# Optimization experiments

Hardware: AMD Instinct MI355X
Metric: run time of the kernel (lower is better)

## Reference

```python
import jax, jax.numpy as jnp
import numpy as np

# Config constants (match init_kwargs)
T = 1024            # num_tokens
H = 2048            # hidden_size
E = 16              # n_routed_experts
I = 1408            # moe_intermediate_size
TOP_K = 4           # num_experts_per_tok
N_GROUP = 4         # n_group
TOPK_GROUP = 2      # topk_group
N_SHARED = 2        # n_shared_experts
SI = I * N_SHARED   # shared intermediate = 2816
ROUTED_SCALE = 1.0  # routed_scaling_factor
RENORMALIZE = True  # norm_topk_prob


def setup_inputs() -> dict:
    key = jax.random.key(0)
    ks = jax.random.split(key, 6)
    scale_w = 0.02  # keep router logits in a sane range
    return {
        "x": jax.random.normal(ks[0], (T, H), dtype=jnp.float32),
        "gate_w": jax.random.normal(ks[1], (E, H), dtype=jnp.float32) * scale_w,
        "w_gate_up": jax.random.normal(ks[2], (E, H, 2 * I), dtype=jnp.float32) * scale_w,
        "w_down": jax.random.normal(ks[3], (E, I, H), dtype=jnp.float32) * scale_w,
        "shared_gate_up": jax.random.normal(ks[4], (H, 2 * SI), dtype=jnp.float32) * scale_w,
        "shared_down": jax.random.normal(ks[5], (SI, H), dtype=jnp.float32) * scale_w,
    }


def _silu_and_mul(gu):
    gate, up = jnp.split(gu, 2, axis=-1)
    return jax.nn.silu(gate) * up


def _grouped_topk(logits):
    # scores over experts, grouped top-k group selection, then top-k experts
    scores = jax.nn.softmax(logits, axis=-1)                          # [T, E]
    group_scores = scores.reshape(T, N_GROUP, E // N_GROUP).max(-1)   # [T, G]
    _, grp_idx = jax.lax.top_k(group_scores, TOPK_GROUP)              # [T, topk_group]
    grp_mask = jnp.zeros((T, N_GROUP), scores.dtype).at[
        jnp.arange(T)[:, None], grp_idx].set(1.0)                     # [T, G]
    score_mask = jnp.repeat(grp_mask, E // N_GROUP, axis=1)           # [T, E]
    tmp = jnp.where(score_mask > 0, scores, 0.0)
    topk_w, topk_ids = jax.lax.top_k(tmp, TOP_K)                      # [T, K]
    if RENORMALIZE:
        topk_w = topk_w / jnp.sum(topk_w, axis=-1, keepdims=True)
    # dense combine-weight matrix [T, E] (top-k ids are distinct per token)
    cw = jnp.zeros((T, E), scores.dtype).at[
        jnp.arange(T)[:, None], topk_ids].set(topk_w)
    return cw


def reference(x, gate_w, w_gate_up, w_down, shared_gate_up, shared_down):
    # shared experts MLP (SiluAndMul)
    shared_out = _silu_and_mul(x @ shared_gate_up) @ shared_down      # [T, H]

    # router
    logits = x @ gate_w.T                                             # [T, E]
    cw = _grouped_topk(logits)                                        # [T, E]

    # routed experts: dense grouped GEMM over all experts, masked combine
    h = jnp.einsum('th,ehi->eti', x, w_gate_up)                       # [E, T, 2I]
    a = _silu_and_mul(h)                                              # [E, T, I]
    y = jnp.einsum('eti,eih->eth', a, w_down)                         # [E, T, H]
    routed = jnp.einsum('eth,te->th', y, cw)                          # [T, H]

    return routed * ROUTED_SCALE + shared_out
```

## Files before the change

kernel.cpp:

```cpp
#include <hip/hip_runtime.h>
#include <hip/hip_bf16.h>
#include <stdint.h>
#include <math.h>

#define T_TOK 1024
#define H_DIM 2048
#define E_NUM 16
#define I_DIM 1408
#define TOPK  4
#define SI_DIM 2816
#define NSLOT (T_TOK * TOPK)

typedef short bf16x8 __attribute__((ext_vector_type(8)));
typedef float f32x4  __attribute__((ext_vector_type(4)));

__device__ __forceinline__ uint32_t fbf(float f) {
  __hip_bfloat16 h = __float2bfloat16(f);
  return (uint32_t)*reinterpret_cast<uint16_t*>(&h);
}
__device__ __forceinline__ float asf(uint32_t u) {
  union { uint32_t u; float f; } c; c.u = u; return c.f;
}

typedef const __attribute__((address_space(1))) char gld_g;
typedef __attribute__((address_space(3))) char gld_l;
__device__ __forceinline__ void gload16(const void* g, void* l) {
  __builtin_amdgcn_global_load_lds((gld_g*)g, (gld_l*)l, 16, 0, 0);
}
__device__ __forceinline__ void barrier_lgkm() {
  asm volatile("s_waitcnt lgkmcnt(0)" ::: "memory");
  __builtin_amdgcn_s_barrier();
  __builtin_amdgcn_sched_barrier(0);
}

__global__ __launch_bounds__(256) void k_router(const float* __restrict__ x,
                                                const float* __restrict__ gw,
                                                int* __restrict__ topk_id,
                                                float* __restrict__ topk_w) {
  int t = blockIdx.x;
  float acc[E_NUM];
#pragma unroll
  for (int e = 0; e < E_NUM; ++e) acc[e] = 0.f;
  for (int h = threadIdx.x; h < H_DIM; h += 256) {
    float xv = x[(long)t * H_DIM + h];
#pragma unroll
    for (int e = 0; e < E_NUM; ++e) acc[e] += xv * gw[e * H_DIM + h];
  }
#pragma unroll
  for (int e = 0; e < E_NUM; ++e) {
#pragma unroll
    for (int off = 32; off; off >>= 1) acc[e] += __shfl_down(acc[e], off);
  }
  __shared__ float part[4][E_NUM];
  int wid = threadIdx.x >> 6, lane = threadIdx.x & 63;
  if (lane == 0) {
#pragma unroll
    for (int e = 0; e < E_NUM; ++e) part[wid][e] = acc[e];
  }
  __syncthreads();
  if (threadIdx.x == 0) {
    float lg[E_NUM], p[E_NUM];
    float m = -1e30f;
    for (int e = 0; e < E_NUM; ++e) {
      lg[e] = part[0][e] + part[1][e] + part[2][e] + part[3][e];
      m = fmaxf(m, lg[e]);
    }
    float s = 0.f;
    for (int e = 0; e < E_NUM; ++e) { p[e] = expf(lg[e] - m); s += p[e]; }
    float inv = 1.f / s;
    for (int e = 0; e < E_NUM; ++e) p[e] *= inv;
    float gs[4];
    for (int g = 0; g < 4; ++g) {
      float mg = p[g * 4];
      for (int i = 1; i < 4; ++i) mg = fmaxf(mg, p[g * 4 + i]);
      gs[g] = mg;
    }
    int g1 = 0;
    for (int g = 1; g < 4; ++g) if (gs[g] > gs[g1]) g1 = g;
    int g2 = -1;
    for (int g = 0; g < 4; ++g) {
      if (g == g1) continue;
      if (g2 < 0 || gs[g] > gs[g2]) g2 = g;
    }
    float q[E_NUM];
    for (int e = 0; e < E_NUM; ++e)
      q[e] = ((e >> 2) == g1 || (e >> 2) == g2) ? p[e] : -1e30f;
    int ids[TOPK]; float wv[TOPK]; float wsum = 0.f;
    for (int k = 0; k < TOPK; ++k) {
      int best = 0; float bv = -2e30f;
      for (int e = 0; e < E_NUM; ++e) if (q[e] > bv) { bv = q[e]; best = e; }
      ids[k] = best; wv[k] = p[best]; wsum += p[best]; q[best] = -3e30f;
    }
    float winv = 1.f / wsum;
    for (int k = 0; k < TOPK; ++k) {
      topk_id[t * TOPK + k] = ids[k];
      topk_w[t * TOPK + k] = wv[k] * winv;
    }
  }
}

__global__ __launch_bounds__(256) void k_count(const int* __restrict__ topk_id,
                                               int* __restrict__ counts) {
  int e = blockIdx.x, tid = threadIdx.x;
  int c = 0;
  for (int s = tid; s < NSLOT; s += 256) c += (topk_id[s] == e);
#pragma unroll
  for (int off = 32; off; off >>= 1) c += __shfl_down(c, off);
  __shared__ int wsum[4];
  int wid = tid >> 6, lane = tid & 63;
  if (lane == 0) wsum[wid] = c;
  __syncthreads();
  if (tid == 0) counts[e] = wsum[0] + wsum[1] + wsum[2] + wsum[3];
}

__global__ void k_offs(const int* __restrict__ counts, int* __restrict__ offs,
                       int* __restrict__ cum) {
  if (threadIdx.x == 0 && blockIdx.x == 0) {
    int s = 0, c = 0;
    cum[0] = 0;
    for (int e = 0; e < E_NUM; ++e) {
      offs[e] = s; s += counts[e];
      c += (counts[e] + 127) >> 7;
      cum[e + 1] = c;
    }
    offs[E_NUM] = s;
  }
}

__global__ __launch_bounds__(256) void k_fill(const int* __restrict__ topk_id,
                                              const int* __restrict__ offs,
                                              int* __restrict__ tok_of_row,
                                              int* __restrict__ row_of_slot) {
  int e = blockIdx.x, tid = threadIdx.x;
  int t0 = tid * 4;
  int match[4]; int cnt = 0;
#pragma unroll
  for (int i = 0; i < 4; ++i) {
    int t = t0 + i; int mk = -1;
#pragma unroll
    for (int k = 0; k < TOPK; ++k) if (topk_id[t * TOPK + k] == e) mk = k;
    match[i] = mk; cnt += (mk >= 0);
  }
  __shared__ int sc[256];
  sc[tid] = cnt; __syncthreads();
  for (int d = 1; d < 256; d <<= 1) {
    int v = sc[tid];
    if (tid >= d) v += sc[tid - d];
    __syncthreads();
    sc[tid] = v;
    __syncthreads();
  }
  int row = offs[e] + sc[tid] - cnt;
#pragma unroll
  for (int i = 0; i < 4; ++i) {
    if (match[i] >= 0) {
      tok_of_row[row] = t0 + i;
      row_of_slot[(t0 + i) * TOPK + match[i]] = row;
      ++row;
    }
  }
}

__global__ __launch_bounds__(256) void k_cvt(const float* __restrict__ in,
                                             uint16_t* __restrict__ out) {
  int i = (blockIdx.x * 256 + threadIdx.x) * 4;
  float4 v = *(const float4*)(in + i);
  uint2 p;
  p.x = fbf(v.x) | (fbf(v.y) << 16);
  p.y = fbf(v.z) | (fbf(v.w) << 16);
  *(uint2*)(out + i) = p;
}

template <int MODE>
__global__ __launch_bounds__(256, 4) void k_gemm(
    const uint16_t* __restrict__ As, int ldas,
    const float* __restrict__ Bs, int ldbs, int upS,
    void* __restrict__ OutS, int ldoS, int NMs, int NNs, int Ks, int f32S,
    const uint16_t* __restrict__ Ar, int ldar,
    const float* __restrict__ Br, int ldbr, long bstr, int upR,
    void* __restrict__ OutR, int ldoR, int NN1, int K1, int f32R,
    const int* __restrict__ offs, const int* __restrict__ rowlist,
    const int* __restrict__ cum) {
  constexpr int BN = (MODE == 0) ? 64 : 128;
  constexpr int NI = (MODE == 0) ? 2 : 4;
  constexpr int BB = 16384;
  constexpr int BMS = 5120;
  __shared__ char smem[26624];

  const int S = NMs * NNs;
  const int NBw = S + cum[E_NUM] * NN1;
  int f = blockIdx.x;
  if (f >= NBw) return;
  int q = NBw >> 3, r = NBw & 7;
  int xcd = f & 7, o = f >> 3;
  int f2 = (xcd < r ? xcd * (q + 1) : r * (q + 1) + (xcd - r) * q) + o;

  const uint16_t* A; const float* Bp; void* Outp; const int* rl;
  int lda, ldb, up, ldo, K, m0, n0, row_end, isf32;
  if (f2 < S) {
    int mb = f2 % NMs, nb = f2 / NMs;
    A = As; lda = ldas; Bp = Bs; ldb = ldbs; up = upS;
    Outp = OutS; ldo = ldoS; K = Ks; isf32 = f32S; rl = nullptr;
    m0 = mb * 128; row_end = NMs * 128; n0 = nb * BN;
  } else {
    int g = f2 - S;
    int e = 0;
    for (e = 0; e < E_NUM; ++e) if (g < cum[e + 1] * NN1) break;
    int nmbe = cum[e + 1] - cum[e];
    int loc = g - cum[e] * NN1;
    int mb = loc % nmbe, nb = loc / nmbe;
    A = Ar; lda = ldar; Bp = Br + (size_t)e * bstr; ldb = ldbr; up = upR;
    Outp = OutR; ldo = ldoR; K = K1; isf32 = f32R; rl = rowlist;
    m0 = offs[e] + mb * 128; row_end = offs[e + 1]; n0 = nb * BN;
  }

  const int tid = threadIdx.x;
  const int wid = tid >> 6, lane = tid & 63;
  const int wm = (wid >> 1) * 64, wn = (wid & 1) * (BN / 2);
  const int lrow = lane & 15, kg = lane >> 4;

  const uint16_t* aSrc[2]; int aDst[2];
#pragma unroll
  for (int p = 0; p < 2; ++p) {
    int rr = wid * 32 + p * 16 + (lane >> 2);
    int grow = m0 + rr;
    grow = grow < row_end - 1 ? grow : row_end - 1;
    int arow = rl ? rl[grow] : grow;
    aSrc[p] = A + (size_t)arow * lda + (lane & 3) * 8;
    aDst[p] = wid * 2048 + p * 1024;
  }

  int n4, kq, mat;
  if constexpr (MODE == 0) {
    n4 = (tid & 15) * 4; int rest = tid >> 4; kq = rest & 7; mat = rest >> 3;
  } else {
    n4 = (tid & 31) * 4; kq = tid >> 5; mat = 0;
  }
  const int k0 = kq * 4;
  const float* bptr = Bp + (size_t)k0 * ldb + n0 + n4 + (mat ? up : 0);
  const int sq = (kq >> 1) & 3, hf = kq & 1;
  int bw[4];
#pragma unroll
  for (int j = 0; j < 4; ++j) {
    int n = n4 + j;
    bw[j] = BB + mat * BMS + n * 80 + ((sq ^ ((n >> 4) & 3)) << 4) + (hf << 3);
  }

  float4 v[4];
  auto loadB = [&]() {
#pragma unroll
    for (int i = 0; i < 4; ++i) v[i] = *(const float4*)(bptr + (size_t)i * ldb);
    bptr += (size_t)32 * ldb;
  };
  auto stageB = [&]() {
#pragma unroll
    for (int j = 0; j < 4; ++j) {
      uint2 w;
      w.x = fbf(((const float*)&v[0])[j]) | (fbf(((const float*)&v[1])[j]) << 16);
      w.y = fbf(((const float*)&v[2])[j]) | (fbf(((const float*)&v[3])[j]) << 16);
      *(uint2*)(smem + bw[j]) = w;
    }
  };

  f32x4 zero = {0.f, 0.f, 0.f, 0.f};
  f32x4 accg[4][NI];
  f32x4 accu[(MODE == 0) ? 4 : 1][(MODE == 0) ? NI : 1];
#pragma unroll
  for (int mi = 0; mi < 4; ++mi)
#pragma unroll
    for (int ni = 0; ni < NI; ++ni) {
      accg[mi][ni] = zero;
      if constexpr (MODE == 0) accu[mi][ni] = zero;
    }

  const int nk = K >> 5;
#pragma unroll
  for (int p = 0; p < 2; ++p) { gload16(aSrc[p], smem + aDst[p]); aSrc[p] += 32; }
  loadB();

  for (int kt = 0; kt < nk; ++kt) {
    const int cur = kt & 1;
    __syncthreads();
    if (kt + 1 < nk) {
#pragma unroll
      for (int p = 0; p < 2; ++p) {
        gload16(aSrc[p], smem + (cur ^ 1) * 8192 + aDst[p]); aSrc[p] += 32;
      }
    }
    stageB();
    if (kt + 1 < nk) loadB();
    barrier_lgkm();

    const char* abuf = smem + cur * 8192;
    bf16x8 af[4];
#pragma unroll
    for (int mi = 0; mi < 4; ++mi)
      af[mi] = *(const bf16x8*)(abuf + (wm + mi * 16 + lrow) * 64 + kg * 16);
#pragma unroll
    for (int ni = 0; ni < NI; ++ni) {
      int n = wn + ni * 16 + lrow;
      int bo = BB + n * 80 + ((kg ^ ((n >> 4) & 3)) << 4);
      bf16x8 bg = *(const bf16x8*)(smem + bo);
#pragma unroll
      for (int mi = 0; mi < 4; ++mi)
        accg[mi][ni] = __builtin_amdgcn_mfma_f32_16x16x32_bf16(
            af[mi], bg, accg[mi][ni], 0, 0, 0);
      if constexpr (MODE == 0) {
        bf16x8 bu = *(const bf16x8*)(smem + bo + BMS);
#pragma unroll
        for (int mi = 0; mi < 4; ++mi)
          accu[mi][ni] = __builtin_amdgcn_mfma_f32_16x16x32_bf16(
              af[mi], bu, accu[mi][ni], 0, 0, 0);
      }
    }
  }

#pragma unroll
  for (int mi = 0; mi < 4; ++mi) {
#pragma unroll
    for (int rr = 0; rr < 4; ++rr) {
      int grow = m0 + wm + mi * 16 + kg * 4 + rr;
      if (grow >= row_end) continue;
#pragma unroll
      for (int ni = 0; ni < NI; ++ni) {
        int col = n0 + wn + ni * 16 + lrow;
        float g = accg[mi][ni][rr];
        if constexpr (MODE == 0) {
          float u = accu[mi][ni][rr];
          float a = g / (1.f + __expf(-g)) * u;
          ((uint16_t*)Outp)[(size_t)grow * ldo + col] = (uint16_t)fbf(a);
        } else {
          if (isf32)
            ((float*)Outp)[(size_t)grow * ldo + col] = g;
          else
            ((uint16_t*)Outp)[(size_t)grow * ldo + col] = (uint16_t)fbf(g);
        }
      }
    }
  }
}

__global__ __launch_bounds__(256) void k_combine(float* __restrict__ out,
    const uint16_t* __restrict__ y, const int* __restrict__ row_of_slot,
    const float* __restrict__ topk_w, const float* __restrict__ p0) {
  int t = blockIdx.x, tid = threadIdx.x;
  int h = tid * 8;
  size_t off = (size_t)t * H_DIM + h;
  float4 o0 = *(const float4*)(p0 + off);
  float4 o1 = *(const float4*)(p0 + off + 4);
#pragma unroll
  for (int k = 0; k < TOPK; ++k) {
    int row = row_of_slot[t * TOPK + k];
    float wk = topk_w[t * TOPK + k];
    uint4 v = *(const uint4*)(y + (size_t)row * H_DIM + h);
    o0.x += wk * asf(v.x << 16); o0.y += wk * asf(v.x & 0xffff0000u);
    o0.z += wk * asf(v.y << 16); o0.w += wk * asf(v.y & 0xffff0000u);
    o1.x += wk * asf(v.z << 16); o1.y += wk * asf(v.z & 0xffff0000u);
    o1.z += wk * asf(v.w << 16); o1.w += wk * asf(v.w & 0xffff0000u);
  }
  *(float4*)(out + off) = o0;
  *(float4*)(out + off + 4) = o1;
}

extern "C" void kernel_launch(void* const* d_in, const int* in_sizes, int n_in,
                              void* d_out, int out_size, void* d_ws,
                              size_t ws_size, hipStream_t stream) {
  const float* x   = (const float*)d_in[0];
  const float* gw  = (const float*)d_in[1];
  const float* wgu = (const float*)d_in[2];
  const float* wd  = (const float*)d_in[3];
  const float* sgu = (const float*)d_in[4];
  const float* sd  = (const float*)d_in[5];
  float* out = (float*)d_out;

  char* ws = (char*)d_ws;
  int*   topk_id     = (int*)(ws + 0);
  float* topk_w      = (float*)(ws + 16384);
  int*   counts      = (int*)(ws + 32768);
  int*   offs        = (int*)(ws + 33792);
  int*   cum         = (int*)(ws + 34816);
  int*   tok_of_row  = (int*)(ws + 35840);
  int*   row_of_slot = (int*)(ws + 52224);
  uint16_t* x_bf     = (uint16_t*)(ws + 131072);
  uint16_t* act      = (uint16_t*)(ws + 4325376);
  uint16_t* yslots   = (uint16_t*)(ws + 15859712);
  uint16_t* act_sh   = (uint16_t*)(ws + 32636928);
  bool merged = ws_size >= (size_t)38404096 + 8388608;
  float* p0 = merged ? (float*)(ws + 38404096) : (float*)(ws + 4325376);

  k_router<<<T_TOK, 256, 0, stream>>>(x, gw, topk_id, topk_w);
  k_count<<<E_NUM, 256, 0, stream>>>(topk_id, counts);
  k_offs<<<1, 1, 0, stream>>>(counts, offs, cum);
  k_fill<<<E_NUM, 256, 0, stream>>>(topk_id, offs, tok_of_row, row_of_slot);
  k_cvt<<<(T_TOK * H_DIM) / 1024, 256, 0, stream>>>(x, x_bf);

  k_gemm<0><<<352 + 48 * 22, 256, 0, stream>>>(
      x_bf, H_DIM, sgu, 2 * SI_DIM, SI_DIM, act_sh, SI_DIM, 8, 44, H_DIM, 0,
      x_bf, H_DIM, wgu, 2 * I_DIM, (long)H_DIM * 2 * I_DIM, I_DIM,
      act, I_DIM, 22, H_DIM, 0,
      offs, tok_of_row, cum);

  if (merged) {
    k_gemm<1><<<128 + 48 * 16, 256, 0, stream>>>(
        act_sh, SI_DIM, sd, H_DIM, 0, p0, H_DIM, 8, 16, SI_DIM, 1,
        act, I_DIM, wd, H_DIM, (long)I_DIM * H_DIM, 0,
        yslots, H_DIM, 16, I_DIM, 0,
        offs, nullptr, cum);
  } else {
    k_gemm<1><<<48 * 16, 256, 0, stream>>>(
        act_sh, SI_DIM, sd, H_DIM, 0, p0, H_DIM, 8, 0, SI_DIM, 1,
        act, I_DIM, wd, H_DIM, (long)I_DIM * H_DIM, 0,
        yslots, H_DIM, 16, I_DIM, 0,
        offs, nullptr, cum);
    k_gemm<1><<<128, 256, 0, stream>>>(
        act_sh, SI_DIM, sd, H_DIM, 0, p0, H_DIM, 8, 16, SI_DIM, 1,
        act, I_DIM, wd, H_DIM, (long)I_DIM * H_DIM, 0,
        yslots, H_DIM, 0, I_DIM, 0,
        offs, nullptr, cum);
  }
  k_combine<<<T_TOK, 256, 0, stream>>>(out, yslots, row_of_slot, topk_w, p0);
}
```

Before: 348.9 us.

## Replace LDS-direct A loads with register-prefetched, double-buffered A/B staging pipeline

The GEMM kernel drops the global_load_lds path for A and loads both A and B tiles through registers. It keeps two k-steps of loads in flight (even and odd register sets) and double-buffers B in LDS, so each k-step needs only one barrier instead of two. A is now XOR-swizzled in LDS to reduce bank conflicts. This raises LDS use and register pressure, so launch bounds drop from 4 to 3 blocks per CU, trading occupancy for deeper software pipelining.

After: 625.1 us. 79.2% more time.

```diff
diff --git a/kernel.cpp b/kernel.cpp
--- a/kernel.cpp
+++ b/kernel.cpp
@@ -22,12 +22,7 @@
   union { uint32_t u; float f; } c; c.u = u; return c.f;
 }
 
-typedef const __attribute__((address_space(1))) char gld_g;
-typedef __attribute__((address_space(3))) char gld_l;
-__device__ __forceinline__ void gload16(const void* g, void* l) {
-  __builtin_amdgcn_global_load_lds((gld_g*)g, (gld_l*)l, 16, 0, 0);
-}
-__device__ __forceinline__ void barrier_lgkm() {
+__device__ __forceinline__ void barrier_stage() {
   asm volatile("s_waitcnt lgkmcnt(0)" ::: "memory");
   __builtin_amdgcn_s_barrier();
   __builtin_amdgcn_sched_barrier(0);
@@ -172,7 +167,7 @@
 }
 
 template <int MODE>
-__global__ __launch_bounds__(256, 4) void k_gemm(
+__global__ __launch_bounds__(256, 3) void k_gemm(
     const uint16_t* __restrict__ As, int ldas,
     const float* __restrict__ Bs, int ldbs, int upS,
     void* __restrict__ OutS, int ldoS, int NMs, int NNs, int Ks, int f32S,
@@ -183,9 +178,8 @@
     const int* __restrict__ cum) {
   constexpr int BN = (MODE == 0) ? 64 : 128;
   constexpr int NI = (MODE == 0) ? 2 : 4;
-  constexpr int BB = 16384;
   constexpr int BMS = 5120;
-  __shared__ char smem[26624];
+  __shared__ char smem[36864];
 
   const int S = NMs * NNs;
   const int NBw = S + cum[E_NUM] * NN1;
@@ -219,15 +213,17 @@
   const int wm = (wid >> 1) * 64, wn = (wid & 1) * (BN / 2);
   const int lrow = lane & 15, kg = lane >> 4;
 
-  const uint16_t* aSrc[2]; int aDst[2];
+  const int ar = tid >> 1;
+  int agr = m0 + ar;
+  agr = agr < row_end - 1 ? agr : row_end - 1;
+  const int arow = rl ? rl[agr] : agr;
+  const uint16_t* aE = A + (size_t)arow * lda + (tid & 1) * 16;
+  const uint16_t* aO = aE + 32;
+  int awOff[2];
 #pragma unroll
   for (int p = 0; p < 2; ++p) {
-    int rr = wid * 32 + p * 16 + (lane >> 2);
-    int grow = m0 + rr;
-    grow = grow < row_end - 1 ? grow : row_end - 1;
-    int arow = rl ? rl[grow] : grow;
-    aSrc[p] = A + (size_t)arow * lda + (lane & 3) * 8;
-    aDst[p] = wid * 2048 + p * 1024;
+    int slot = ((tid & 1) * 2 + p) ^ ((ar >> 1) & 3);
+    awOff[p] = ar * 64 + slot * 16;
   }
 
   int n4, kq, mat;
@@ -237,28 +233,43 @@
     n4 = (tid & 31) * 4; kq = tid >> 5; mat = 0;
   }
   const int k0 = kq * 4;
-  const float* bptr = Bp + (size_t)k0 * ldb + n0 + n4 + (mat ? up : 0);
+  const float* bE = Bp + (size_t)k0 * ldb + n0 + n4 + (mat ? up : 0);
+  const float* bO = bE + (size_t)32 * ldb;
   const int sq = (kq >> 1) & 3, hf = kq & 1;
-  int bw[4];
+  int bwOff[4];
 #pragma unroll
   for (int j = 0; j < 4; ++j) {
     int n = n4 + j;
-    bw[j] = BB + mat * BMS + n * 80 + ((sq ^ ((n >> 4) & 3)) << 4) + (hf << 3);
-  }
-
-  float4 v[4];
-  auto loadB = [&]() {
-#pragma unroll
-    for (int i = 0; i < 4; ++i) v[i] = *(const float4*)(bptr + (size_t)i * ldb);
-    bptr += (size_t)32 * ldb;
+    bwOff[j] = mat * BMS + n * 80 + ((sq ^ ((n >> 4) & 3)) << 4) + (hf << 3);
+  }
+
+  uint4 av0[2], av1[2];
+  float4 bv0[4], bv1[4];
+  auto issueE = [&](uint4 (&av)[2], float4 (&bv)[4]) {
+    av[0] = *(const uint4*)aE; av[1] = *(const uint4*)(aE + 8); aE += 64;
+#pragma unroll
+    for (int i = 0; i < 4; ++i) bv[i] = *(const float4*)(bE + (size_t)i * ldb);
+    bE += (size_t)64 * ldb;
   };
-  auto stageB = [&]() {
-#pragma unroll
-    for (int j = 0; j < 4; ++j) {
+  auto issueO = [&](uint4 (&av)[2], float4 (&bv)[4]) {
+    av[0] = *(const uint4*)aO; av[1] = *(const uint4*)(aO + 8); aO += 64;
+#pragma unroll
+    for (int i = 0; i < 4; ++i) bv[i] = *(const float4*)(bO + (size_t)i * ldb);
+    bO += (size_t)64 * ldb;
+  };
+  auto stage = [&](int j, uint4 (&av)[2], float4 (&bv)[4]) {
+    char* ab = smem + (j & 1) * 8192;
+    char* bb = smem + 16384 + (j & 1) * 10240;
+    *(uint4*)(ab + awOff[0]) = av[0];
+    *(uint4*)(ab + awOff[1]) = av[1];
+#pragma unroll
+    for (int jj = 0; jj < 4; ++jj) {
       uint2 w;
-      w.x = fbf(((const float*)&v[0])[j]) | (fbf(((const float*)&v[1])[j]) << 16);
-      w.y = fbf(((const float*)&v[2])[j]) | (fbf(((const float*)&v[3])[j]) << 16);
-      *(uint2*)(smem + bw[j]) = w;
+      w.x = fbf(((const float*)&bv[0])[jj]) |
+            (fbf(((const float*)&bv[1])[jj]) << 16);
+      w.y = fbf(((const float*)&bv[2])[jj]) |
+            (fbf(((const float*)&bv[3])[jj]) << 16);
+      *(uint2*)(bb + bwOff[jj]) = w;
     }
   };
 
@@ -273,44 +284,54 @@
       if constexpr (MODE == 0) accu[mi][ni] = zero;
     }
 
-  const int nk = K >> 5;
-#pragma unroll
-  for (int p = 0; p < 2; ++p) { gload16(aSrc[p], smem + aDst[p]); aSrc[p] += 32; }
-  loadB();
-
-  for (int kt = 0; kt < nk; ++kt) {
-    const int cur = kt & 1;
-    __syncthreads();
-    if (kt + 1 < nk) {
-#pragma unroll
-      for (int p = 0; p < 2; ++p) {
-        gload16(aSrc[p], smem + (cur ^ 1) * 8192 + aDst[p]); aSrc[p] += 32;
-      }
-    }
-    stageB();
-    if (kt + 1 < nk) loadB();
-    barrier_lgkm();
-
-    const char* abuf = smem + cur * 8192;
+  auto compute = [&](int j) {
+    const char* ab = smem + (j & 1) * 8192;
+    const char* bb = smem + 16384 + (j & 1) * 10240;
     bf16x8 af[4];
 #pragma unroll
-    for (int mi = 0; mi < 4; ++mi)
-      af[mi] = *(const bf16x8*)(abuf + (wm + mi * 16 + lrow) * 64 + kg * 16);
+    for (int mi = 0; mi < 4; ++mi) {
+      int row = wm + mi * 16 + lrow;
+      af[mi] = *(const bf16x8*)(ab + row * 64 +
+                                ((kg ^ ((lrow >> 1) & 3)) << 4));
+    }
 #pragma unroll
     for (int ni = 0; ni < NI; ++ni) {
       int n = wn + ni * 16 + lrow;
-      int bo = BB + n * 80 + ((kg ^ ((n >> 4) & 3)) << 4);
-      bf16x8 bg = *(const bf16x8*)(smem + bo);
+      int bo = n * 80 + ((kg ^ ((n >> 4) & 3)) << 4);
+      bf16x8 bg = *(const bf16x8*)(bb + bo);
 #pragma unroll
       for (int mi = 0; mi < 4; ++mi)
         accg[mi][ni] = __builtin_amdgcn_mfma_f32_16x16x32_bf16(
             af[mi], bg, accg[mi][ni], 0, 0, 0);
       if constexpr (MODE == 0) {
-        bf16x8 bu = *(const bf16x8*)(smem + bo + BMS);
+        bf16x8 bu = *(const bf16x8*)(bb + bo + BMS);
 #pragma unroll
         for (int mi = 0; mi < 4; ++mi)
           accu[mi][ni] = __builtin_amdgcn_mfma_f32_16x16x32_bf16(
               af[mi], bu, accu[mi][ni], 0, 0, 0);
+      }
+    }
+  };
+
+  const int nk = K >> 5;
+  issueE(av0, bv0);
+  issueO(av1, bv1);
+  stage(0, av0, bv0);
+  barrier_stage();
+
+  for (int kt = 0; kt < nk; kt += 2) {
+    if (kt + 2 < nk) issueE(av0, bv0);
+    compute(kt);
+    if (kt + 1 < nk) {
+      stage(kt + 1, av1, bv1);
+      barrier_stage();
+    }
+    if (kt + 3 < nk) issueO(av1, bv1);
+    if (kt + 1 < nk) {
+      compute(kt + 1);
+      if (kt + 2 < nk) {
+        stage(kt + 2, av0, bv0);
+        barrier_stage();
       }
     }
   }
```

## Deepen GEMM pipeline to triple-buffered A tiles with two-ahead B register prefetch

Applied to the files above, without the earlier changes.

Restructures the GEMM main loop so A tiles use three LDS buffers and B fp32 tiles are prefetched two k-steps ahead into alternating register sets, using explicit vmcnt waits in place of a full sync per step. The goal is to hide more global load latency behind MFMA work. In exchange, shared memory grows to about 34KB, extra registers hold the second B prefetch, and the MODE 1 occupancy hint drops to 3 blocks per CU. The hand-written waitcnt counts must match the number of outstanding loads exactly, otherwise the loop reads stale data.

Result: slower. 394.8 us (+13.2%).

```diff
diff --git a/kernel.cpp b/kernel.cpp
--- a/kernel.cpp
+++ b/kernel.cpp
@@ -26,11 +26,6 @@
 typedef __attribute__((address_space(3))) char gld_l;
 __device__ __forceinline__ void gload16(const void* g, void* l) {
   __builtin_amdgcn_global_load_lds((gld_g*)g, (gld_l*)l, 16, 0, 0);
-}
-__device__ __forceinline__ void barrier_lgkm() {
-  asm volatile("s_waitcnt lgkmcnt(0)" ::: "memory");
-  __builtin_amdgcn_s_barrier();
-  __builtin_amdgcn_sched_barrier(0);
 }
 
 __global__ __launch_bounds__(256) void k_router(const float* __restrict__ x,
@@ -172,7 +167,7 @@
 }
 
 template <int MODE>
-__global__ __launch_bounds__(256, 4) void k_gemm(
+__global__ __launch_bounds__(256, (MODE == 0) ? 4 : 3) void k_gemm(
     const uint16_t* __restrict__ As, int ldas,
     const float* __restrict__ Bs, int ldbs, int upS,
     void* __restrict__ OutS, int ldoS, int NMs, int NNs, int Ks, int f32S,
@@ -183,9 +178,9 @@
     const int* __restrict__ cum) {
   constexpr int BN = (MODE == 0) ? 64 : 128;
   constexpr int NI = (MODE == 0) ? 2 : 4;
-  constexpr int BB = 16384;
+  constexpr int BB = 24576;
   constexpr int BMS = 5120;
-  __shared__ char smem[26624];
+  __shared__ char smem[34816];
 
   const int S = NMs * NNs;
   const int NBw = S + cum[E_NUM] * NN1;
@@ -246,18 +241,23 @@
     bw[j] = BB + mat * BMS + n * 80 + ((sq ^ ((n >> 4) & 3)) << 4) + (hf << 3);
   }
 
-  float4 v[4];
-  auto loadB = [&]() {
-#pragma unroll
-    for (int i = 0; i < 4; ++i) v[i] = *(const float4*)(bptr + (size_t)i * ldb);
+  float4 bvE[4], bvO[4];
+  auto issue = [&](int bufIdx, float4 (&bv)[4]) {
+    char* ab = smem + bufIdx * 8192;
+#pragma unroll
+    for (int p = 0; p < 2; ++p) { gload16(aSrc[p], ab + aDst[p]); aSrc[p] += 32; }
+#pragma unroll
+    for (int i = 0; i < 4; ++i) bv[i] = *(const float4*)(bptr + (size_t)i * ldb);
     bptr += (size_t)32 * ldb;
   };
-  auto stageB = [&]() {
+  auto stageB = [&](float4 (&bv)[4]) {
 #pragma unroll
     for (int j = 0; j < 4; ++j) {
       uint2 w;
-      w.x = fbf(((const float*)&v[0])[j]) | (fbf(((const float*)&v[1])[j]) << 16);
-      w.y = fbf(((const float*)&v[2])[j]) | (fbf(((const float*)&v[3])[j]) << 16);
+      w.x = fbf(((const float*)&bv[0])[j]) |
+            (fbf(((const float*)&bv[1])[j]) << 16);
+      w.y = fbf(((const float*)&bv[2])[j]) |
+            (fbf(((const float*)&bv[3])[j]) << 16);
       *(uint2*)(smem + bw[j]) = w;
     }
   };
@@ -273,29 +273,12 @@
       if constexpr (MODE == 0) accu[mi][ni] = zero;
     }
 
-  const int nk = K >> 5;
-#pragma unroll
-  for (int p = 0; p < 2; ++p) { gload16(aSrc[p], smem + aDst[p]); aSrc[p] += 32; }
-  loadB();
-
-  for (int kt = 0; kt < nk; ++kt) {
-    const int cur = kt & 1;
-    __syncthreads();
-    if (kt + 1 < nk) {
-#pragma unroll
-      for (int p = 0; p < 2; ++p) {
-        gload16(aSrc[p], smem + (cur ^ 1) * 8192 + aDst[p]); aSrc[p] += 32;
-      }
-    }
-    stageB();
-    if (kt + 1 < nk) loadB();
-    barrier_lgkm();
-
-    const char* abuf = smem + cur * 8192;
+  auto compute = [&](int bufIdx) {
+    const char* ab = smem + bufIdx * 8192;
     bf16x8 af[4];
 #pragma unroll
     for (int mi = 0; mi < 4; ++mi)
-      af[mi] = *(const bf16x8*)(abuf + (wm + mi * 16 + lrow) * 64 + kg * 16);
+      af[mi] = *(const bf16x8*)(ab + (wm + mi * 16 + lrow) * 64 + kg * 16);
 #pragma unroll
     for (int ni = 0; ni < NI; ++ni) {
       int n = wn + ni * 16 + lrow;
@@ -312,6 +295,45 @@
           accu[mi][ni] = __builtin_amdgcn_mfma_f32_16x16x32_bf16(
               af[mi], bu, accu[mi][ni], 0, 0, 0);
       }
+    }
+  };
+
+  const int nk = K >> 5;
+  issue(0, bvE);
+  issue(1, bvO);
+
+  int bi = 0;
+  for (int kt = 0; kt < nk; kt += 2) {
+    if (kt + 1 < nk) asm volatile("s_waitcnt vmcnt(6)" ::: "memory");
+    else             asm volatile("s_waitcnt vmcnt(0)" ::: "memory");
+    __builtin_amdgcn_s_barrier();
+    __builtin_amdgcn_sched_barrier(0);
+    stageB(bvE);
+    {
+      int tgt = bi + 2; if (tgt >= 3) tgt -= 3;
+      if (kt + 2 < nk) issue(tgt, bvE);
+    }
+    asm volatile("s_waitcnt lgkmcnt(0)" ::: "memory");
+    __builtin_amdgcn_s_barrier();
+    __builtin_amdgcn_sched_barrier(0);
+    compute(bi);
+    bi = (bi + 1 == 3) ? 0 : bi + 1;
+
+    if (kt + 1 < nk) {
+      if (kt + 2 < nk) asm volatile("s_waitcnt vmcnt(6)" ::: "memory");
+      else             asm volatile("s_waitcnt vmcnt(0)" ::: "memory");
+      __builtin_amdgcn_s_barrier();
+      __builtin_amdgcn_sched_barrier(0);
+      stageB(bvO);
+      {
+        int tgt = bi + 2; if (tgt >= 3) tgt -= 3;
+        if (kt + 3 < nk) issue(tgt, bvO);
+      }
+      asm volatile("s_waitcnt lgkmcnt(0)" ::: "memory");
+      __builtin_amdgcn_s_barrier();
+      __builtin_amdgcn_sched_barrier(0);
+      compute(bi);
+      bi = (bi + 1 == 3) ? 0 : bi + 1;
     }
   }
 
```

## Double GEMM M-tile to 256 rows and swizzle A shared-memory layout

Applied to the files above, without the earlier changes.

Each block of the grouped GEMM now covers 256 rows instead of 128, so every B (weight) tile is converted from fp32 and staged once for twice as many MFMAs. This halves the number of blocks and the repeated weight reads. The A tile in shared memory is now XOR-swizzled to avoid bank conflicts. The larger tile doubles accumulator registers and shared memory, and occupancy drops to 2 blocks per CU. Experts with few tokens waste more padded rows, and fewer blocks may underfill the 256 CUs.

Measured after the change: 322.1 us, median of 8. 7.7% less time.

```diff
diff --git a/kernel.cpp b/kernel.cpp
--- a/kernel.cpp
+++ b/kernel.cpp
@@ -120,7 +120,7 @@
     cum[0] = 0;
     for (int e = 0; e < E_NUM; ++e) {
       offs[e] = s; s += counts[e];
-      c += (counts[e] + 127) >> 7;
+      c += (counts[e] + 255) >> 8;
       cum[e + 1] = c;
     }
     offs[E_NUM] = s;
@@ -172,7 +172,7 @@
 }
 
 template <int MODE>
-__global__ __launch_bounds__(256, 4) void k_gemm(
+__global__ __launch_bounds__(256, 2) void k_gemm(
     const uint16_t* __restrict__ As, int ldas,
     const float* __restrict__ Bs, int ldbs, int upS,
     void* __restrict__ OutS, int ldoS, int NMs, int NNs, int Ks, int f32S,
@@ -183,9 +183,9 @@
     const int* __restrict__ cum) {
   constexpr int BN = (MODE == 0) ? 64 : 128;
   constexpr int NI = (MODE == 0) ? 2 : 4;
-  constexpr int BB = 16384;
+  constexpr int BB = 32768;
   constexpr int BMS = 5120;
-  __shared__ char smem[26624];
+  __shared__ char smem[43008];
 
   const int S = NMs * NNs;
   const int NBw = S + cum[E_NUM] * NN1;
@@ -201,17 +201,18 @@
     int mb = f2 % NMs, nb = f2 / NMs;
     A = As; lda = ldas; Bp = Bs; ldb = ldbs; up = upS;
     Outp = OutS; ldo = ldoS; K = Ks; isf32 = f32S; rl = nullptr;
-    m0 = mb * 128; row_end = NMs * 128; n0 = nb * BN;
+    m0 = mb * 256; row_end = NMs * 256; n0 = nb * BN;
   } else {
     int g = f2 - S;
     int e = 0;
     for (e = 0; e < E_NUM; ++e) if (g < cum[e + 1] * NN1) break;
+    if (e == E_NUM) return;
     int nmbe = cum[e + 1] - cum[e];
     int loc = g - cum[e] * NN1;
     int mb = loc % nmbe, nb = loc / nmbe;
     A = Ar; lda = ldar; Bp = Br + (size_t)e * bstr; ldb = ldbr; up = upR;
     Outp = OutR; ldo = ldoR; K = K1; isf32 = f32R; rl = rowlist;
-    m0 = offs[e] + mb * 128; row_end = offs[e + 1]; n0 = nb * BN;
+    m0 = offs[e] + mb * 256; row_end = offs[e + 1]; n0 = nb * BN;
   }
 
   const int tid = threadIdx.x;
@@ -219,15 +220,16 @@
   const int wm = (wid >> 1) * 64, wn = (wid & 1) * (BN / 2);
   const int lrow = lane & 15, kg = lane >> 4;
 
-  const uint16_t* aSrc[2]; int aDst[2];
-#pragma unroll
-  for (int p = 0; p < 2; ++p) {
-    int rr = wid * 32 + p * 16 + (lane >> 2);
+  const uint16_t* aSrc[4]; int aDst[4];
+#pragma unroll
+  for (int p = 0; p < 4; ++p) {
+    int rr = wid * 64 + p * 16 + (lane >> 2);
     int grow = m0 + rr;
     grow = grow < row_end - 1 ? grow : row_end - 1;
     int arow = rl ? rl[grow] : grow;
-    aSrc[p] = A + (size_t)arow * lda + (lane & 3) * 8;
-    aDst[p] = wid * 2048 + p * 1024;
+    int sslot = (lane & 3) ^ ((lane >> 3) & 3);
+    aSrc[p] = A + (size_t)arow * lda + sslot * 8;
+    aDst[p] = wid * 4096 + p * 1024;
   }
 
   int n4, kq, mat;
@@ -263,19 +265,55 @@
   };
 
   f32x4 zero = {0.f, 0.f, 0.f, 0.f};
-  f32x4 accg[4][NI];
-  f32x4 accu[(MODE == 0) ? 4 : 1][(MODE == 0) ? NI : 1];
-#pragma unroll
-  for (int mi = 0; mi < 4; ++mi)
+  f32x4 accg[2][4][NI];
+  f32x4 accu[(MODE == 0) ? 2 : 1][(MODE == 0) ? 4 : 1][(MODE == 0) ? NI : 1];
+#pragma unroll
+  for (int mt = 0; mt < 2; ++mt)
+#pragma unroll
+    for (int mi = 0; mi < 4; ++mi)
+#pragma unroll
+      for (int ni = 0; ni < NI; ++ni) {
+        accg[mt][mi][ni] = zero;
+        if constexpr (MODE == 0) accu[mt][mi][ni] = zero;
+      }
+
+  auto compute = [&](int cur) {
+    const char* ab = smem + cur * 16384;
+    const int akx = (kg ^ ((lrow >> 1) & 3)) << 4;
+    bf16x8 af[8];
+#pragma unroll
+    for (int mt = 0; mt < 2; ++mt)
+#pragma unroll
+      for (int mi = 0; mi < 4; ++mi) {
+        int row = mt * 128 + wm + mi * 16 + lrow;
+        af[mt * 4 + mi] = *(const bf16x8*)(ab + row * 64 + akx);
+      }
 #pragma unroll
     for (int ni = 0; ni < NI; ++ni) {
-      accg[mi][ni] = zero;
-      if constexpr (MODE == 0) accu[mi][ni] = zero;
-    }
+      int n = wn + ni * 16 + lrow;
+      int bo = BB + n * 80 + ((kg ^ ((n >> 4) & 3)) << 4);
+      bf16x8 bg = *(const bf16x8*)(smem + bo);
+#pragma unroll
+      for (int mt = 0; mt < 2; ++mt)
+#pragma unroll
+        for (int mi = 0; mi < 4; ++mi)
+          accg[mt][mi][ni] = __builtin_amdgcn_mfma_f32_16x16x32_bf16(
+              af[mt * 4 + mi], bg, accg[mt][mi][ni], 0, 0, 0);
+      if constexpr (MODE == 0) {
+        bf16x8 bu = *(const bf16x8*)(smem + bo + BMS);
+#pragma unroll
+        for (int mt = 0; mt < 2; ++mt)
+#pragma unroll
+          for (int mi = 0; mi < 4; ++mi)
+            accu[mt][mi][ni] = __builtin_amdgcn_mfma_f32_16x16x32_bf16(
+                af[mt * 4 + mi], bu, accu[mt][mi][ni], 0, 0, 0);
+      }
+    }
+  };
 
   const int nk = K >> 5;
 #pragma unroll
-  for (int p = 0; p < 2; ++p) { gload16(aSrc[p], smem + aDst[p]); aSrc[p] += 32; }
+  for (int p = 0; p < 4; ++p) { gload16(aSrc[p], smem + aDst[p]); aSrc[p] += 32; }
   loadB();
 
   for (int kt = 0; kt < nk; ++kt) {
@@ -283,57 +321,38 @@
     __syncthreads();
     if (kt + 1 < nk) {
 #pragma unroll
-      for (int p = 0; p < 2; ++p) {
-        gload16(aSrc[p], smem + (cur ^ 1) * 8192 + aDst[p]); aSrc[p] += 32;
+      for (int p = 0; p < 4; ++p) {
+        gload16(aSrc[p], smem + (cur ^ 1) * 16384 + aDst[p]); aSrc[p] += 32;
       }
     }
     stageB();
     if (kt + 1 < nk) loadB();
     barrier_lgkm();
-
-    const char* abuf = smem + cur * 8192;
-    bf16x8 af[4];
-#pragma unroll
-    for (int mi = 0; mi < 4; ++mi)
-      af[mi] = *(const bf16x8*)(abuf + (wm + mi * 16 + lrow) * 64 + kg * 16);
-#pragma unroll
-    for (int ni = 0; ni < NI; ++ni) {
-      int n = wn + ni * 16 + lrow;
-      int bo = BB + n * 80 + ((kg ^ ((n >> 4) & 3)) << 4);
-      bf16x8 bg = *(const bf16x8*)(smem + bo);
-#pragma unroll
-      for (int mi = 0; mi < 4; ++mi)
-        accg[mi][ni] = __builtin_amdgcn_mfma_f32_16x16x32_bf16(
-            af[mi], bg, accg[mi][ni], 0, 0, 0);
-      if constexpr (MODE == 0) {
-        bf16x8 bu = *(const bf16x8*)(smem + bo + BMS);
-#pragma unroll
-        for (int mi = 0; mi < 4; ++mi)
-          accu[mi][ni] = __builtin_amdgcn_mfma_f32_16x16x32_bf16(
-              af[mi], bu, accu[mi][ni], 0, 0, 0);
-      }
-    }
-  }
-
-#pragma unroll
-  for (int mi = 0; mi < 4; ++mi) {
-#pragma unroll
-    for (int rr = 0; rr < 4; ++rr) {
-      int grow = m0 + wm + mi * 16 + kg * 4 + rr;
-      if (grow >= row_end) continue;
-#pragma unroll
-      for (int ni = 0; ni < NI; ++ni) {
-        int col = n0 + wn + ni * 16 + lrow;
-        float g = accg[mi][ni][rr];
-        if constexpr (MODE == 0) {
-          float u = accu[mi][ni][rr];
-          float a = g / (1.f + __expf(-g)) * u;
-          ((uint16_t*)Outp)[(size_t)grow * ldo + col] = (uint16_t)fbf(a);
-        } else {
-          if (isf32)
-            ((float*)Outp)[(size_t)grow * ldo + col] = g;
-          else
-            ((uint16_t*)Outp)[(size_t)grow * ldo + col] = (uint16_t)fbf(g);
+    compute(cur);
+  }
+
+#pragma unroll
+  for (int mt = 0; mt < 2; ++mt) {
+#pragma unroll
+    for (int mi = 0; mi < 4; ++mi) {
+#pragma unroll
+      for (int rr = 0; rr < 4; ++rr) {
+        int grow = m0 + mt * 128 + wm + mi * 16 + kg * 4 + rr;
+        if (grow >= row_end) continue;
+#pragma unroll
+        for (int ni = 0; ni < NI; ++ni) {
+          int col = n0 + wn + ni * 16 + lrow;
+          float g = accg[mt][mi][ni][rr];
+          if constexpr (MODE == 0) {
+            float u = accu[mt][mi][ni][rr];
+            float a = g / (1.f + __expf(-g)) * u;
+            ((uint16_t*)Outp)[(size_t)grow * ldo + col] = (uint16_t)fbf(a);
+          } else {
+            if (isf32)
+              ((float*)Outp)[(size_t)grow * ldo + col] = g;
+            else
+              ((uint16_t*)Outp)[(size_t)grow * ldo + col] = (uint16_t)fbf(g);
+          }
         }
       }
     }
@@ -394,26 +413,26 @@
   k_fill<<<E_NUM, 256, 0, stream>>>(topk_id, offs, tok_of_row, row_of_slot);
   k_cvt<<<(T_TOK * H_DIM) / 1024, 256, 0, stream>>>(x, x_bf);
 
-  k_gemm<0><<<352 + 48 * 22, 256, 0, stream>>>(
-      x_bf, H_DIM, sgu, 2 * SI_DIM, SI_DIM, act_sh, SI_DIM, 8, 44, H_DIM, 0,
+  k_gemm<0><<<176 + 32 * 22, 256, 0, stream>>>(
+      x_bf, H_DIM, sgu, 2 * SI_DIM, SI_DIM, act_sh, SI_DIM, 4, 44, H_DIM, 0,
       x_bf, H_DIM, wgu, 2 * I_DIM, (long)H_DIM * 2 * I_DIM, I_DIM,
       act, I_DIM, 22, H_DIM, 0,
       offs, tok_of_row, cum);
 
   if (merged) {
-    k_gemm<1><<<128 + 48 * 16, 256, 0, stream>>>(
-        act_sh, SI_DIM, sd, H_DIM, 0, p0, H_DIM, 8, 16, SI_DIM, 1,
+    k_gemm<1><<<64 + 32 * 16, 256, 0, stream>>>(
+        act_sh, SI_DIM, sd, H_DIM, 0, p0, H_DIM, 4, 16, SI_DIM, 1,
         act, I_DIM, wd, H_DIM, (long)I_DIM * H_DIM, 0,
         yslots, H_DIM, 16, I_DIM, 0,
         offs, nullptr, cum);
   } else {
-    k_gemm<1><<<48 * 16, 256, 0, stream>>>(
-        act_sh, SI_DIM, sd, H_DIM, 0, p0, H_DIM, 8, 0, SI_DIM, 1,
+    k_gemm<1><<<32 * 16, 256, 0, stream>>>(
+        act_sh, SI_DIM, sd, H_DIM, 0, p0, H_DIM, 4, 0, SI_DIM, 1,
         act, I_DIM, wd, H_DIM, (long)I_DIM * H_DIM, 0,
         yslots, H_DIM, 16, I_DIM, 0,
         offs, nullptr, cum);
-    k_gemm<1><<<128, 256, 0, stream>>>(
-        act_sh, SI_DIM, sd, H_DIM, 0, p0, H_DIM, 8, 16, SI_DIM, 1,
+    k_gemm<1><<<64, 256, 0, stream>>>(
+        act_sh, SI_DIM, sd, H_DIM, 0, p0, H_DIM, 4, 16, SI_DIM, 1,
         act, I_DIM, wd, H_DIM, (long)I_DIM * H_DIM, 0,
         yslots, H_DIM, 0, I_DIM, 0,
         offs, nullptr, cum);
```
